# Kernel optimization log

Measured on AMD Instinct MI355X. Metric: run time of the kernel, lower is better.

Reference implementation:

```python
import jax, jax.numpy as jnp
import numpy as np

K_NEIGHBORS = 32
BN_EPS = 1e-5


def setup_inputs() -> dict:
    key = jax.random.key(0)
    ks = jax.random.split(key, 5)
    B, N, C, OUT = 16, 2048, 3, 32
    x = jax.random.normal(ks[0], (B, N, C), dtype=jnp.float32)
    W1 = jax.random.normal(ks[1], (2 * C, 2 * C), dtype=jnp.float32) * 0.3
    b1 = jax.random.normal(ks[2], (2 * C,), dtype=jnp.float32) * 0.05
    W2 = jax.random.normal(ks[3], (2 * C, OUT), dtype=jnp.float32) * 0.3
    b2 = jax.random.normal(ks[4], (OUT,), dtype=jnp.float32) * 0.05
    return {
        "x": x,
        "W1": W1, "b1": b1,
        "gamma1": jnp.ones((2 * C,), jnp.float32), "beta1": jnp.zeros((2 * C,), jnp.float32),
        "W2": W2, "b2": b2,
        "gamma2": jnp.ones((OUT,), jnp.float32), "beta2": jnp.zeros((OUT,), jnp.float32),
    }


def _batchnorm_train(h, gamma, beta):
    # normalize over all axes except the last (channel) axis, biased variance
    axes = tuple(range(h.ndim - 1))
    mean = jnp.mean(h, axis=axes)
    var = jnp.var(h, axis=axes)
    return gamma * (h - mean) * jax.lax.rsqrt(var + BN_EPS) + beta


def reference(x, W1, b1, gamma1, beta1, W2, b2, gamma2, beta2):
    B, N, C = x.shape
    K = min(K_NEIGHBORS, N)
    # brute-force KNN: squared euclidean distances [B,N,N]
    sq = jnp.sum(x * x, axis=-1)
    d = sq[:, :, None] + sq[:, None, :] - 2.0 * jnp.einsum('bnc,bmc->bnm', x, x)
    _, idx = jax.lax.top_k(-d, K)  # [B,N,K] nearest (self first)
    # gather neighbor points: [B,N,K,C]
    knn = jax.vmap(lambda pts, i: pts[i])(x, idx)
    diffs = x[:, :, None, :] - knn
    h = jnp.concatenate([jnp.broadcast_to(x[:, :, None, :], (B, N, K, C)), diffs], axis=-1)  # [B,N,K,2C]
    h = jax.nn.elu(_batchnorm_train(h @ W1 + b1, gamma1, beta1))
    h = jnp.max(h, axis=2)  # max-pool over K neighbors -> [B,N,2C]
    y = jax.nn.elu(_batchnorm_train(h @ W2 + b2, gamma2, beta2))
    return y
```

## Files before the change

kernel.cpp:

```cpp
#include <hip/hip_runtime.h>
#include <math.h>

namespace {
constexpr int NB = 16, NP = 2048, KNN = 32, CH1 = 6, CH2 = 32;
constexpr int NBLK = NB * NP / 8;
constexpr float BN_EPS = 1e-5f;

constexpr size_t OFF_STATS2 = 0;
constexpr size_t OFF_SC1    = 512;
constexpr size_t OFF_P      = 1024;
constexpr size_t OFF_MINQ   = OFF_P    + sizeof(float)*NB*NP*CH1;
constexpr size_t OFF_PART   = OFF_MINQ + sizeof(float)*NB*NP*CH1;
}

template <int C> __device__ __forceinline__ int dpp0i(int x) {
  return __builtin_amdgcn_update_dpp(0, x, C, 0xf, 0xf, true);
}
template <int C> __device__ __forceinline__ float dpp0f(float x) {
  return __uint_as_float((unsigned)__builtin_amdgcn_update_dpp(
      0, (int)__float_as_uint(x), C, 0xf, 0xf, true));
}
template <int C> __device__ __forceinline__ float dppInff(float x) {
  return __uint_as_float((unsigned)__builtin_amdgcn_update_dpp(
      0x7F800000, (int)__float_as_uint(x), C, 0xf, 0xf, false));
}
__device__ __forceinline__ int wave_isum_bcast(int x) {
  x += dpp0i<0x111>(x); x += dpp0i<0x112>(x); x += dpp0i<0x114>(x);
  x += dpp0i<0x118>(x); x += dpp0i<0x142>(x); x += dpp0i<0x143>(x);
  return __builtin_amdgcn_readlane(x, 63);
}
__device__ __forceinline__ float wave_fsum63(float x) {
  x += dpp0f<0x111>(x); x += dpp0f<0x112>(x); x += dpp0f<0x114>(x);
  x += dpp0f<0x118>(x); x += dpp0f<0x142>(x); x += dpp0f<0x143>(x);
  return x;
}
__device__ __forceinline__ float wave_fmin63(float x) {
  x = fminf(x, dppInff<0x111>(x)); x = fminf(x, dppInff<0x112>(x));
  x = fminf(x, dppInff<0x114>(x)); x = fminf(x, dppInff<0x118>(x));
  x = fminf(x, dppInff<0x142>(x)); x = fminf(x, dppInff<0x143>(x));
  return x;
}

#define BSEL(m, x, y) ((((x)) & (m)) | (((y)) & ~(m)))

__global__ __launch_bounds__(512, 6) void knn_kernel(const float* __restrict__ x,
                                                     const float* __restrict__ W1,
                                                     const float* __restrict__ b1,
                                                     float* __restrict__ pout,
                                                     float* __restrict__ minq,
                                                     float* __restrict__ part) {
  __shared__ float4 pts[NP];
  __shared__ float red[12][8];
  const int lane = threadIdx.x & 63;
  const int w    = threadIdx.x >> 6;
  const int qi   = blockIdx.x * 8 + w;
  const int b    = qi >> 11;
  const int n    = qi & (NP - 1);

  const float* xb = x + (size_t)b * NP * 3;
  for (int j = threadIdx.x; j < NP; j += 512) {
    float a0 = xb[j*3+0], a1 = xb[j*3+1], a2 = xb[j*3+2];
    float sq = __fadd_rn(__fadd_rn(__fmul_rn(a0,a0), __fmul_rn(a1,a1)), __fmul_rn(a2,a2));
    pts[j] = make_float4(a0, a1, a2, sq);
  }
  __syncthreads();

  const float4 xq = pts[n];

  unsigned a[32];
#pragma unroll
  for (int t = 0; t < 32; ++t) {
    float4 pj = pts[t*64 + lane];
    float dot = __fadd_rn(__fadd_rn(__fmul_rn(xq.x,pj.x), __fmul_rn(xq.y,pj.y)),
                          __fmul_rn(xq.z,pj.z));
    float d = __fsub_rn(__fadd_rn(xq.w, pj.w), __fmul_rn(2.0f, dot));
    a[31 - t] = __float_as_uint(d) | 0x80000000u;
  }

#pragma unroll
  for (int g = 0; g < 16; ++g) {
    unsigned hi = a[g], lo = a[g+16];
    a[g]    = __builtin_amdgcn_perm(hi, lo, 0x07060302u);
    a[g+16] = __builtin_amdgcn_perm(hi, lo, 0x05040100u);
  }
#pragma unroll
  for (int g = 0; g < 16; ++g) {
    int k = (g >> 3)*16 + (g & 7);
    unsigned hi = a[k], lo = a[k+8];
    a[k]   = __builtin_amdgcn_perm(hi, lo, 0x07030501u);
    a[k+8] = __builtin_amdgcn_perm(hi, lo, 0x06020400u);
  }
#pragma unroll
  for (int g = 0; g < 16; ++g) {
    int k = (g >> 2)*8 + (g & 3);
    unsigned A = a[k], B = a[k+4];
    a[k]   = BSEL(0x0F0F0F0Fu, B >> 4, A);
    a[k+4] = BSEL(0xF0F0F0F0u, A << 4, B);
  }
#pragma unroll
  for (int g = 0; g < 16; ++g) {
    int k = (g >> 1)*4 + (g & 1);
    unsigned A = a[k], B = a[k+2];
    a[k]   = BSEL(0x33333333u, B >> 2, A);
    a[k+2] = BSEL(0xCCCCCCCCu, A << 2, B);
  }
#pragma unroll
  for (int g = 0; g < 16; ++g) {
    int k = g*2;
    unsigned A = a[k], B = a[k+1];
    a[k]   = BSEL(0x55555555u, B >> 1, A);
    a[k+1] = BSEL(0xAAAAAAAAu, A << 1, B);
  }

  unsigned alive = 0xFFFFFFFFu, below = 0u;
  int rem = KNN;
#pragma unroll
  for (int i = 1; i <= 15; ++i) {
    unsigned zeros = alive & ~a[i];
    int c0 = wave_isum_bcast(__popc(zeros));
    if (c0 >= rem) alive = zeros;
    else { rem -= c0; below |= zeros; alive &= a[i]; }
  }
  int ca = wave_isum_bcast(__popc(alive));
#pragma unroll
  for (int i = 16; i < 32; ++i) {
    if (ca != rem) {
      unsigned zeros = alive & ~a[i];
      int c0 = wave_isum_bcast(__popc(zeros));
      if (c0 >= rem) { alive = zeros; ca = c0; }
      else { rem -= c0; below |= zeros; alive &= a[i]; ca -= c0; }
    }
  }
  unsigned sel = below;
  if (ca == rem) {
    sel |= alive;
  } else {
    for (int v = 0; v < 32; ++v) {
      if (rem <= 0) break;
      bool mine = (alive >> v) & 1;
      unsigned long long m = __ballot(mine);
      int c = __popcll(m);
      if (c <= rem) { if (mine) sel |= 1u << v; rem -= c; }
      else {
        if (mine && (int)__popcll(m & ((1ull << lane) - 1)) < rem) sel |= 1u << v;
        rem = 0;
      }
    }
  }

  float sq_[CH1], sqq[CH1], mn[CH1];
#pragma unroll
  for (int c = 0; c < CH1; ++c) { sq_[c] = 0.f; sqq[c] = 0.f; mn[c] = INFINITY; }
  unsigned m = sel;
  while (m) {
    int v = __builtin_ctz(m); m &= m - 1;
    float4 pj = pts[(v << 6) | lane];
#pragma unroll
    for (int c = 0; c < CH1; ++c) {
      float qv = pj.x*W1[3*CH1+c] + pj.y*W1[4*CH1+c] + pj.z*W1[5*CH1+c];
      sq_[c] += qv; sqq[c] += qv*qv; mn[c] = fminf(mn[c], qv);
    }
  }

  float pv[CH1];
#pragma unroll
  for (int c = 0; c < CH1; ++c) {
    float qv = xq.x*W1[3*CH1+c] + xq.y*W1[4*CH1+c] + xq.z*W1[5*CH1+c];
    pv[c] = b1[c] + xq.x*W1[c] + xq.y*W1[CH1+c] + xq.z*W1[2*CH1+c] + qv;
  }

#pragma unroll
  for (int c = 0; c < CH1; ++c) {
    float s  = wave_fsum63(sq_[c]);
    float s2 = wave_fsum63(sqq[c]);
    float mm = wave_fmin63(mn[c]);
    if (lane == 63) {
      minq[qi*CH1 + c] = mm;
      float hs = fmaf(32.f, pv[c], -s);
      float hq = fmaf(32.f, pv[c]*pv[c], fmaf(-2.f*pv[c], s, s2));
      red[c][w] = hs; red[CH1 + c][w] = hq;
    }
  }
  if (lane == 0) {
#pragma unroll
    for (int c = 0; c < CH1; ++c) pout[qi*CH1 + c] = pv[c];
  }
  __syncthreads();
  if (threadIdx.x < 12) {
    float s = 0.f;
#pragma unroll
    for (int ww = 0; ww < 8; ++ww) s += red[threadIdx.x][ww];
    part[threadIdx.x * NBLK + blockIdx.x] = s;
  }
}

__global__ __launch_bounds__(768) void reduce_fin1_kernel(const float* __restrict__ part,
                                                          const float* __restrict__ gamma1,
                                                          const float* __restrict__ beta1,
                                                          float* __restrict__ sc1) {
  __shared__ float tot[12];
  const int lane = threadIdx.x & 63, w = threadIdx.x >> 6;
  float s = 0.f;
  for (int it = 0; it < NBLK / 64; ++it) s += part[w * NBLK + it * 64 + lane];
  s = wave_fsum63(s);
  if (lane == 63) tot[w] = s;
  __syncthreads();
  if (threadIdx.x < CH1) {
    int c = threadIdx.x;
    double cnt  = (double)NB * NP * KNN;
    double mean = (double)tot[c] / cnt;
    double var  = (double)tot[CH1 + c] / cnt - mean * mean;
    float vf    = (float)var + BN_EPS;
    float scale = gamma1[c] / sqrtf(vf);
    sc1[c]        = scale;
    sc1[CH1 + c]  = beta1[c] - (float)mean * scale;
  }
}

__global__ __launch_bounds__(256) void stage2_kernel(const float* __restrict__ p,
                                                     const float* __restrict__ minq,
                                                     const float* __restrict__ sc1,
                                                     const float* __restrict__ W2,
                                                     const float* __restrict__ b2,
                                                     double* __restrict__ stats2) {
  __shared__ float rs[4][CH2], rq[4][CH2];
  const int qi = blockIdx.x * 256 + threadIdx.x;
  const int w = threadIdx.x >> 6, lane = threadIdx.x & 63;
  float me[CH1];
#pragma unroll
  for (int c = 0; c < CH1; ++c) {
    float mval = p[qi*CH1 + c] - minq[qi*CH1 + c];
    float t = fmaf(sc1[c], mval, sc1[CH1 + c]);
    me[c] = t > 0.f ? t : expm1f(t);
  }
#pragma unroll
  for (int o = 0; o < CH2; ++o) {
    float y = b2[o];
#pragma unroll
    for (int c = 0; c < CH1; ++c) y = fmaf(me[c], W2[c*CH2 + o], y);
    float s  = wave_fsum63(y);
    float s2 = wave_fsum63(y * y);
    if (lane == 63) { rs[w][o] = s; rq[w][o] = s2; }
  }
  __syncthreads();
  if (threadIdx.x < CH2) {
    int o = threadIdx.x;
    atomicAdd(stats2 + o, (double)((rs[0][o] + rs[1][o]) + (rs[2][o] + rs[3][o])));
  } else if (threadIdx.x < 2*CH2) {
    int o = threadIdx.x - CH2;
    atomicAdd(stats2 + CH2 + o, (double)((rq[0][o] + rq[1][o]) + (rq[2][o] + rq[3][o])));
  }
}

__global__ __launch_bounds__(256) void out_kernel(const float* __restrict__ p,
                                                  const float* __restrict__ minq,
                                                  const float* __restrict__ sc1,
                                                  const float* __restrict__ W2,
                                                  const float* __restrict__ b2,
                                                  const double* __restrict__ stats2,
                                                  const float* __restrict__ gamma2,
                                                  const float* __restrict__ beta2,
                                                  float* __restrict__ out) {
  __shared__ float me_lds[8][CH1];
  __shared__ float s2s[CH2], s2h[CH2];
  const int t = threadIdx.x;
  if (t < CH2) {
    double cnt  = (double)NB * NP;
    double mean = stats2[t] / cnt;
    double var  = stats2[CH2 + t] / cnt - mean * mean;
    float vf    = (float)var + BN_EPS;
    float scale = gamma2[t] / sqrtf(vf);
    s2s[t] = scale; s2h[t] = beta2[t] - (float)mean * scale;
  }
  const int qbase = blockIdx.x * 8;
  if (t < 48) {
    int qs = t / 6, c = t % 6;
    int qi = qbase + qs;
    float mval = p[qi*CH1 + c] - minq[qi*CH1 + c];
    float v = fmaf(sc1[c], mval, sc1[CH1 + c]);
    me_lds[qs][c] = v > 0.f ? v : expm1f(v);
  }
  __syncthreads();
  const int qs = t >> 5, o = t & 31;
  const int qi = qbase + qs;
  float y = b2[o];
#pragma unroll
  for (int c = 0; c < CH1; ++c) y = fmaf(me_lds[qs][c], W2[c*CH2 + o], y);
  float r = fmaf(s2s[o], y, s2h[o]);
  out[(size_t)qi*CH2 + o] = r > 0.f ? r : expm1f(r);
}

extern "C" void kernel_launch(void* const* d_in, const int* in_sizes, int n_in,
                              void* d_out, int out_size, void* d_ws, size_t ws_size,
                              hipStream_t stream) {
  const float* x      = (const float*)d_in[0];
  const float* W1     = (const float*)d_in[1];
  const float* b1     = (const float*)d_in[2];
  const float* gamma1 = (const float*)d_in[3];
  const float* beta1  = (const float*)d_in[4];
  const float* W2     = (const float*)d_in[5];
  const float* b2     = (const float*)d_in[6];
  const float* gamma2 = (const float*)d_in[7];
  const float* beta2  = (const float*)d_in[8];
  float* out = (float*)d_out;
  char* ws = (char*)d_ws;

  double* stats2 = (double*)(ws + OFF_STATS2);
  float* sc1  = (float*)(ws + OFF_SC1);
  float* p    = (float*)(ws + OFF_P);
  float* minq = (float*)(ws + OFF_MINQ);
  float* part = (float*)(ws + OFF_PART);

  hipMemsetAsync(ws, 0, 512, stream);

  knn_kernel       <<<dim3(NBLK),         dim3(512), 0, stream>>>(x, W1, b1, p, minq, part);
  reduce_fin1_kernel<<<dim3(1),           dim3(768), 0, stream>>>(part, gamma1, beta1, sc1);
  stage2_kernel    <<<dim3(NB*NP/256),    dim3(256), 0, stream>>>(p, minq, sc1, W2, b2, stats2);
  out_kernel       <<<dim3(NB*NP/8),      dim3(256), 0, stream>>>(p, minq, sc1, W2, b2,
                                                                  stats2, gamma2, beta2, out);
}
```

Before: 79.06 us.

## Lazy bit-transpose of low distance bits, 16-query blocks, fuse BN1 finalize into stage2

```diff
diff --git a/kernel.cpp b/kernel.cpp
--- a/kernel.cpp
+++ b/kernel.cpp
@@ -3,14 +3,15 @@
 
 namespace {
 constexpr int NB = 16, NP = 2048, KNN = 32, CH1 = 6, CH2 = 32;
-constexpr int NBLK = NB * NP / 8;
+constexpr int QPB = 16;
+constexpr int NBLK = NB * NP / QPB;
 constexpr float BN_EPS = 1e-5f;
 
-constexpr size_t OFF_STATS2 = 0;
-constexpr size_t OFF_SC1    = 512;
-constexpr size_t OFF_P      = 1024;
-constexpr size_t OFF_MINQ   = OFF_P    + sizeof(float)*NB*NP*CH1;
-constexpr size_t OFF_PART   = OFF_MINQ + sizeof(float)*NB*NP*CH1;
+constexpr size_t OFF_S1REP  = 0;
+constexpr size_t OFF_STATS2 = 768;
+constexpr size_t OFF_SC1    = 1280;
+constexpr size_t OFF_P      = 2048;
+constexpr size_t OFF_MINQ   = OFF_P + sizeof(float)*NB*NP*CH1;
 }
 
 template <int C> __device__ __forceinline__ int dpp0i(int x) {
@@ -43,22 +44,22 @@
 
 #define BSEL(m, x, y) ((((x)) & (m)) | (((y)) & ~(m)))
 
-__global__ __launch_bounds__(512, 6) void knn_kernel(const float* __restrict__ x,
-                                                     const float* __restrict__ W1,
-                                                     const float* __restrict__ b1,
-                                                     float* __restrict__ pout,
-                                                     float* __restrict__ minq,
-                                                     float* __restrict__ part) {
+__global__ __launch_bounds__(1024, 8) void knn_kernel(const float* __restrict__ x,
+                                                      const float* __restrict__ W1,
+                                                      const float* __restrict__ b1,
+                                                      float* __restrict__ pout,
+                                                      float* __restrict__ minq,
+                                                      double* __restrict__ s1rep) {
   __shared__ float4 pts[NP];
-  __shared__ float red[12][8];
+  __shared__ float red[12][QPB];
   const int lane = threadIdx.x & 63;
   const int w    = threadIdx.x >> 6;
-  const int qi   = blockIdx.x * 8 + w;
+  const int qi   = blockIdx.x * QPB + w;
   const int b    = qi >> 11;
   const int n    = qi & (NP - 1);
 
   const float* xb = x + (size_t)b * NP * 3;
-  for (int j = threadIdx.x; j < NP; j += 512) {
+  for (int j = threadIdx.x; j < NP; j += 1024) {
     float a0 = xb[j*3+0], a1 = xb[j*3+1], a2 = xb[j*3+2];
     float sq = __fadd_rn(__fadd_rn(__fmul_rn(a0,a0), __fmul_rn(a1,a1)), __fmul_rn(a2,a2));
     pts[j] = make_float4(a0, a1, a2, sq);
@@ -74,7 +75,7 @@
     float dot = __fadd_rn(__fadd_rn(__fmul_rn(xq.x,pj.x), __fmul_rn(xq.y,pj.y)),
                           __fmul_rn(xq.z,pj.z));
     float d = __fsub_rn(__fadd_rn(xq.w, pj.w), __fmul_rn(2.0f, dot));
-    a[31 - t] = __float_as_uint(d) | 0x80000000u;
+    a[31 - t] = __float_as_uint(d);
   }
 
 #pragma unroll
@@ -84,28 +85,27 @@
     a[g+16] = __builtin_amdgcn_perm(hi, lo, 0x05040100u);
   }
 #pragma unroll
-  for (int g = 0; g < 16; ++g) {
-    int k = (g >> 3)*16 + (g & 7);
-    unsigned hi = a[k], lo = a[k+8];
-    a[k]   = __builtin_amdgcn_perm(hi, lo, 0x07030501u);
-    a[k+8] = __builtin_amdgcn_perm(hi, lo, 0x06020400u);
-  }
-#pragma unroll
-  for (int g = 0; g < 16; ++g) {
+  for (int g = 0; g < 8; ++g) {
+    unsigned hi = a[g], lo = a[g+8];
+    a[g]   = __builtin_amdgcn_perm(hi, lo, 0x07030501u);
+    a[g+8] = __builtin_amdgcn_perm(hi, lo, 0x06020400u);
+  }
+#pragma unroll
+  for (int g = 0; g < 8; ++g) {
     int k = (g >> 2)*8 + (g & 3);
     unsigned A = a[k], B = a[k+4];
     a[k]   = BSEL(0x0F0F0F0Fu, B >> 4, A);
     a[k+4] = BSEL(0xF0F0F0F0u, A << 4, B);
   }
 #pragma unroll
-  for (int g = 0; g < 16; ++g) {
+  for (int g = 0; g < 8; ++g) {
     int k = (g >> 1)*4 + (g & 1);
     unsigned A = a[k], B = a[k+2];
     a[k]   = BSEL(0x33333333u, B >> 2, A);
     a[k+2] = BSEL(0xCCCCCCCCu, A << 2, B);
   }
 #pragma unroll
-  for (int g = 0; g < 16; ++g) {
+  for (int g = 0; g < 8; ++g) {
     int k = g*2;
     unsigned A = a[k], B = a[k+1];
     a[k]   = BSEL(0x55555555u, B >> 1, A);
@@ -113,41 +113,75 @@
   }
 
   unsigned alive = 0xFFFFFFFFu, below = 0u;
-  int rem = KNN;
+  int rem = KNN, ca = 2048;
 #pragma unroll
   for (int i = 1; i <= 15; ++i) {
     unsigned zeros = alive & ~a[i];
     int c0 = wave_isum_bcast(__popc(zeros));
-    if (c0 >= rem) alive = zeros;
-    else { rem -= c0; below |= zeros; alive &= a[i]; }
-  }
-  int ca = wave_isum_bcast(__popc(alive));
-#pragma unroll
-  for (int i = 16; i < 32; ++i) {
-    if (ca != rem) {
-      unsigned zeros = alive & ~a[i];
-      int c0 = wave_isum_bcast(__popc(zeros));
-      if (c0 >= rem) { alive = zeros; ca = c0; }
-      else { rem -= c0; below |= zeros; alive &= a[i]; ca -= c0; }
-    }
+    if (c0 >= rem) { alive = zeros; ca = c0; }
+    else { rem -= c0; below |= zeros; alive &= a[i]; ca -= c0; }
   }
   unsigned sel = below;
   if (ca == rem) {
     sel |= alive;
   } else {
-    for (int v = 0; v < 32; ++v) {
-      if (rem <= 0) break;
-      bool mine = (alive >> v) & 1;
-      unsigned long long m = __ballot(mine);
-      int c = __popcll(m);
-      if (c <= rem) { if (mine) sel |= 1u << v; rem -= c; }
-      else {
-        if (mine && (int)__popcll(m & ((1ull << lane) - 1)) < rem) sel |= 1u << v;
-        rem = 0;
+#pragma unroll
+    for (int g = 0; g < 8; ++g) {
+      unsigned hi = a[16+g], lo = a[24+g];
+      a[16+g] = __builtin_amdgcn_perm(hi, lo, 0x07030501u);
+      a[24+g] = __builtin_amdgcn_perm(hi, lo, 0x06020400u);
+    }
+#pragma unroll
+    for (int g = 0; g < 8; ++g) {
+      int k = 16 + (g >> 2)*8 + (g & 3);
+      unsigned A = a[k], B = a[k+4];
+      a[k]   = BSEL(0x0F0F0F0Fu, B >> 4, A);
+      a[k+4] = BSEL(0xF0F0F0F0u, A << 4, B);
+    }
+#pragma unroll
+    for (int g = 0; g < 8; ++g) {
+      int k = 16 + (g >> 1)*4 + (g & 1);
+      unsigned A = a[k], B = a[k+2];
+      a[k]   = BSEL(0x33333333u, B >> 2, A);
+      a[k+2] = BSEL(0xCCCCCCCCu, A << 2, B);
+    }
+#pragma unroll
+    for (int g = 0; g < 8; ++g) {
+      int k = 16 + g*2;
+      unsigned A = a[k], B = a[k+1];
+      a[k]   = BSEL(0x55555555u, B >> 1, A);
+      a[k+1] = BSEL(0xAAAAAAAAu, A << 1, B);
+    }
+#pragma unroll
+    for (int i = 16; i < 32; ++i) {
+      if (ca != rem) {
+        unsigned zeros = alive & ~a[i];
+        int c0 = wave_isum_bcast(__popc(zeros));
+        if (c0 >= rem) { alive = zeros; ca = c0; }
+        else { rem -= c0; below |= zeros; alive &= a[i]; ca -= c0; }
       }
     }
-  }
-
+    sel = below;
+    if (ca == rem) {
+      sel |= alive;
+    } else {
+      for (int v = 0; v < 32; ++v) {
+        if (rem <= 0) break;
+        bool mine = (alive >> v) & 1;
+        unsigned long long mb = __ballot(mine);
+        int c = __popcll(mb);
+        if (c <= rem) { if (mine) sel |= 1u << v; rem -= c; }
+        else {
+          if (mine && (int)__popcll(mb & ((1ull << lane) - 1)) < rem) sel |= 1u << v;
+          rem = 0;
+        }
+      }
+    }
+  }
+
+  float w3[CH1], w4[CH1], w5[CH1];
+#pragma unroll
+  for (int c = 0; c < CH1; ++c) { w3[c]=W1[3*CH1+c]; w4[c]=W1[4*CH1+c]; w5[c]=W1[5*CH1+c]; }
   float sq_[CH1], sqq[CH1], mn[CH1];
 #pragma unroll
   for (int c = 0; c < CH1; ++c) { sq_[c] = 0.f; sqq[c] = 0.f; mn[c] = INFINITY; }
@@ -157,7 +191,7 @@
     float4 pj = pts[(v << 6) | lane];
 #pragma unroll
     for (int c = 0; c < CH1; ++c) {
-      float qv = pj.x*W1[3*CH1+c] + pj.y*W1[4*CH1+c] + pj.z*W1[5*CH1+c];
+      float qv = pj.x*w3[c] + pj.y*w4[c] + pj.z*w5[c];
       sq_[c] += qv; sqq[c] += qv*qv; mn[c] = fminf(mn[c], qv);
     }
   }
@@ -165,7 +199,7 @@
   float pv[CH1];
 #pragma unroll
   for (int c = 0; c < CH1; ++c) {
-    float qv = xq.x*W1[3*CH1+c] + xq.y*W1[4*CH1+c] + xq.z*W1[5*CH1+c];
+    float qv = xq.x*w3[c] + xq.y*w4[c] + xq.z*w5[c];
     pv[c] = b1[c] + xq.x*W1[c] + xq.y*W1[CH1+c] + xq.z*W1[2*CH1+c] + qv;
   }
 
@@ -176,9 +210,8 @@
     float mm = wave_fmin63(mn[c]);
     if (lane == 63) {
       minq[qi*CH1 + c] = mm;
-      float hs = fmaf(32.f, pv[c], -s);
-      float hq = fmaf(32.f, pv[c]*pv[c], fmaf(-2.f*pv[c], s, s2));
-      red[c][w] = hs; red[CH1 + c][w] = hq;
+      red[c][w]       = fmaf(32.f, pv[c], -s);
+      red[CH1 + c][w] = fmaf(32.f, pv[c]*pv[c], fmaf(-2.f*pv[c], s, s2));
     }
   }
   if (lane == 0) {
@@ -189,49 +222,48 @@
   if (threadIdx.x < 12) {
     float s = 0.f;
 #pragma unroll
-    for (int ww = 0; ww < 8; ++ww) s += red[threadIdx.x][ww];
-    part[threadIdx.x * NBLK + blockIdx.x] = s;
-  }
-}
-
-__global__ __launch_bounds__(768) void reduce_fin1_kernel(const float* __restrict__ part,
-                                                          const float* __restrict__ gamma1,
-                                                          const float* __restrict__ beta1,
-                                                          float* __restrict__ sc1) {
-  __shared__ float tot[12];
-  const int lane = threadIdx.x & 63, w = threadIdx.x >> 6;
-  float s = 0.f;
-  for (int it = 0; it < NBLK / 64; ++it) s += part[w * NBLK + it * 64 + lane];
-  s = wave_fsum63(s);
-  if (lane == 63) tot[w] = s;
-  __syncthreads();
-  if (threadIdx.x < CH1) {
-    int c = threadIdx.x;
-    double cnt  = (double)NB * NP * KNN;
-    double mean = (double)tot[c] / cnt;
-    double var  = (double)tot[CH1 + c] / cnt - mean * mean;
-    float vf    = (float)var + BN_EPS;
-    float scale = gamma1[c] / sqrtf(vf);
-    sc1[c]        = scale;
-    sc1[CH1 + c]  = beta1[c] - (float)mean * scale;
-  }
-}
-
-__global__ __launch_bounds__(256) void stage2_kernel(const float* __restrict__ p,
+    for (int ww = 0; ww < QPB; ++ww) s += red[threadIdx.x][ww];
+    atomicAdd(s1rep + (blockIdx.x & 7) * 12 + threadIdx.x, (double)s);
+  }
+}
+
+__global__ __launch_bounds__(128) void stage2_kernel(const float* __restrict__ p,
                                                      const float* __restrict__ minq,
-                                                     const float* __restrict__ sc1,
+                                                     const double* __restrict__ s1rep,
+                                                     const float* __restrict__ gamma1,
+                                                     const float* __restrict__ beta1,
                                                      const float* __restrict__ W2,
                                                      const float* __restrict__ b2,
+                                                     float* __restrict__ sc1g,
                                                      double* __restrict__ stats2) {
-  __shared__ float rs[4][CH2], rq[4][CH2];
-  const int qi = blockIdx.x * 256 + threadIdx.x;
-  const int w = threadIdx.x >> 6, lane = threadIdx.x & 63;
+  __shared__ double tot1[12];
+  __shared__ float sc1s[12];
+  __shared__ float rs[2][CH2], rq[2][CH2];
+  const int t = threadIdx.x;
+  if (t < 12) {
+    double s = 0.0;
+#pragma unroll
+    for (int r = 0; r < 8; ++r) s += s1rep[r*12 + t];
+    tot1[t] = s;
+  }
+  __syncthreads();
+  if (t < CH1) {
+    double cnt  = (double)NB * NP * KNN;
+    double mean = tot1[t] / cnt;
+    double var  = tot1[CH1 + t] / cnt - mean * mean;
+    float scale = gamma1[t] / sqrtf((float)var + BN_EPS);
+    sc1s[t] = scale; sc1s[CH1 + t] = beta1[t] - (float)mean * scale;
+  }
+  __syncthreads();
+  if (blockIdx.x == 0 && t < 12) sc1g[t] = sc1s[t];
+
+  const int qi = blockIdx.x * 128 + t;
+  const int w = t >> 6, lane = t & 63;
   float me[CH1];
 #pragma unroll
   for (int c = 0; c < CH1; ++c) {
-    float mval = p[qi*CH1 + c] - minq[qi*CH1 + c];
-    float t = fmaf(sc1[c], mval, sc1[CH1 + c]);
-    me[c] = t > 0.f ? t : expm1f(t);
+    float v = fmaf(sc1s[c], p[qi*CH1 + c] - minq[qi*CH1 + c], sc1s[CH1 + c]);
+    me[c] = v > 0.f ? v : expm1f(v);
   }
 #pragma unroll
   for (int o = 0; o < CH2; ++o) {
@@ -243,13 +275,8 @@
     if (lane == 63) { rs[w][o] = s; rq[w][o] = s2; }
   }
   __syncthreads();
-  if (threadIdx.x < CH2) {
-    int o = threadIdx.x;
-    atomicAdd(stats2 + o, (double)((rs[0][o] + rs[1][o]) + (rs[2][o] + rs[3][o])));
-  } else if (threadIdx.x < 2*CH2) {
-    int o = threadIdx.x - CH2;
-    atomicAdd(stats2 + CH2 + o, (double)((rq[0][o] + rq[1][o]) + (rq[2][o] + rq[3][o])));
-  }
+  if (t < CH2) atomicAdd(stats2 + t, (double)(rs[0][t] + rs[1][t]));
+  else if (t < 2*CH2) atomicAdd(stats2 + t, (double)(rq[0][t-CH2] + rq[1][t-CH2]));
 }
 
 __global__ __launch_bounds__(256) void out_kernel(const float* __restrict__ p,
@@ -268,16 +295,14 @@
     double cnt  = (double)NB * NP;
     double mean = stats2[t] / cnt;
     double var  = stats2[CH2 + t] / cnt - mean * mean;
-    float vf    = (float)var + BN_EPS;
-    float scale = gamma2[t] / sqrtf(vf);
+    float scale = gamma2[t] / sqrtf((float)var + BN_EPS);
     s2s[t] = scale; s2h[t] = beta2[t] - (float)mean * scale;
   }
   const int qbase = blockIdx.x * 8;
   if (t < 48) {
     int qs = t / 6, c = t % 6;
     int qi = qbase + qs;
-    float mval = p[qi*CH1 + c] - minq[qi*CH1 + c];
-    float v = fmaf(sc1[c], mval, sc1[CH1 + c]);
+    float v = fmaf(sc1[c], p[qi*CH1 + c] - minq[qi*CH1 + c], sc1[CH1 + c]);
     me_lds[qs][c] = v > 0.f ? v : expm1f(v);
   }
   __syncthreads();
@@ -305,17 +330,17 @@
   float* out = (float*)d_out;
   char* ws = (char*)d_ws;
 
+  double* s1rep  = (double*)(ws + OFF_S1REP);
   double* stats2 = (double*)(ws + OFF_STATS2);
   float* sc1  = (float*)(ws + OFF_SC1);
   float* p    = (float*)(ws + OFF_P);
   float* minq = (float*)(ws + OFF_MINQ);
-  float* part = (float*)(ws + OFF_PART);
-
-  hipMemsetAsync(ws, 0, 512, stream);
-
-  knn_kernel       <<<dim3(NBLK),         dim3(512), 0, stream>>>(x, W1, b1, p, minq, part);
-  reduce_fin1_kernel<<<dim3(1),           dim3(768), 0, stream>>>(part, gamma1, beta1, sc1);
-  stage2_kernel    <<<dim3(NB*NP/256),    dim3(256), 0, stream>>>(p, minq, sc1, W2, b2, stats2);
-  out_kernel       <<<dim3(NB*NP/8),      dim3(256), 0, stream>>>(p, minq, sc1, W2, b2,
-                                                                  stats2, gamma2, beta2, out);
-}
+
+  hipMemsetAsync(ws, 0, 1280, stream);
+
+  knn_kernel   <<<dim3(NBLK),       dim3(1024), 0, stream>>>(x, W1, b1, p, minq, s1rep);
+  stage2_kernel<<<dim3(NB*NP/128),  dim3(128),  0, stream>>>(p, minq, s1rep, gamma1, beta1,
+                                                             W2, b2, sc1, stats2);
+  out_kernel   <<<dim3(NB*NP/8),    dim3(256),  0, stream>>>(p, minq, sc1, W2, b2,
+                                                             stats2, gamma2, beta2, out);
+}
```

Measured after the change: 292.6 us. +270.1%, slower.
